# Optimization experiments

Hardware: AMD Instinct MI355X
Metric: run time of the kernel (lower is better)

## Reference

```python
import jax, jax.numpy as jnp
import numpy as np

N_ATOMS = 4096
N_EDGES = 131072
NUM_ELEMENTS = 100
NUM_BESSEL = 8
CUTOFF = 6.0
D_NODE = 64
D_MSG = 128
SH_DIM = 9            # l=0,1,2 -> 1+3+5
TP_IN = D_MSG * SH_DIM  # 1152
N_HEADS = 4
HEAD_DIM = D_MSG // N_HEADS


def setup_inputs() -> dict:
    key = jax.random.key(0)
    ks = jax.random.split(key, 20)
    def p(k, shape):
        return jax.random.normal(k, shape, dtype=jnp.float32) * 0.05
    z = lambda n: jnp.zeros((n,), jnp.float32)
    return {
        "atomic_numbers": jax.random.randint(ks[0], (N_ATOMS,), 0, NUM_ELEMENTS),
        "positions": jax.random.normal(ks[1], (N_ATOMS, 3), dtype=jnp.float32),
        "edge_index": jax.random.randint(ks[2], (2, N_EDGES), 0, N_ATOMS),
        "edge_vectors": jax.random.normal(ks[3], (N_EDGES, 3), dtype=jnp.float32),
        "edge_lengths": jax.random.uniform(ks[4], (N_EDGES,), dtype=jnp.float32, minval=0.5, maxval=5.5),
        "embed_table": p(ks[5], (NUM_ELEMENTS, D_NODE)),
        "W_r1": p(ks[6], (NUM_BESSEL, 64)), "b_r1": z(64),
        "W_r2": p(ks[7], (64, D_MSG)), "b_r2": z(D_MSG),
        "W_tp": p(ks[8], (TP_IN, D_MSG)), "b_tp": z(D_MSG),
        "W_m1": p(ks[9], (D_MSG, D_MSG)), "b_m1": z(D_MSG),
        "W_m2": p(ks[10], (D_MSG, D_MSG)), "b_m2": z(D_MSG),
        "W_qkv": p(ks[11], (D_MSG, 3 * D_MSG)), "b_qkv": z(3 * D_MSG),
        "W_ao": p(ks[12], (D_MSG, D_MSG)), "b_ao": z(D_MSG),
        "W_g": p(ks[13], (D_MSG, D_MSG)), "b_g": z(D_MSG),
        "W_o": p(ks[14], (D_MSG, D_MSG)), "b_o": z(D_MSG),
    }


def reference(atomic_numbers, positions, edge_index, edge_vectors, edge_lengths,
              embed_table, W_r1, b_r1, W_r2, b_r2, W_tp, b_tp,
              W_m1, b_m1, W_m2, b_m2, W_qkv, b_qkv, W_ao, b_ao,
              W_g, b_g, W_o, b_o):
    node_features = embed_table[atomic_numbers]  # [N, 64]

    # spherical harmonics (l = 0,1,2 -> 9 features), order as in source
    r = jnp.linalg.norm(edge_vectors, axis=-1, keepdims=True) + 1e-8
    u = edge_vectors / r
    x, y, z = u[:, 0], u[:, 1], u[:, 2]
    sh = jnp.stack([jnp.ones_like(x), y, z, x,
                    3.0 * z * z - 1.0, x * z, y * z, x * y, x * x - y * y], axis=-1)  # [E,9]

    # bessel RBF with cosine cutoff envelope
    freqs = jnp.arange(1, NUM_BESSEL + 1, dtype=jnp.float32) * (np.pi / CUTOFF)
    env = 0.5 * (jnp.cos(edge_lengths * (np.pi / CUTOFF)) + 1.0) * (edge_lengths < CUTOFF).astype(jnp.float32)
    rbf = jnp.sin(edge_lengths[:, None] * freqs) / edge_lengths[:, None] * env[:, None]  # [E,8]

    radial = jax.nn.silu(rbf @ W_r1 + b_r1)
    radial = jax.nn.silu(radial @ W_r2 + b_r2)  # [E,128]

    # per-edge outer product radial x sh, flattened per-l blocks then concatenated
    outer = radial[:, :, None] * sh[:, None, :]  # [E,128,9]
    E = outer.shape[0]
    edge_messages = jnp.concatenate([
        outer[:, :, 0:1].reshape(E, -1),   # l=0 -> 128
        outer[:, :, 1:4].reshape(E, -1),   # l=1 -> 384
        outer[:, :, 4:9].reshape(E, -1),   # l=2 -> 640
    ], axis=-1)                            # [E,1152]
    edge_messages = edge_messages @ W_tp + b_tp  # [E,128]

    # scatter-add aggregation onto destination nodes (index_add_)
    dst = edge_index[1]
    aggregated = jnp.zeros((node_features.shape[0], D_MSG), jnp.float32).at[dst].add(edge_messages)

    combined = jnp.concatenate([node_features, aggregated[:, :D_NODE]], axis=-1)  # [N,128]
    updated = jax.nn.silu(combined @ W_m1 + b_m1) @ W_m2 + b_m2                   # [N,128]

    # multi-head self-attention over all atoms (batch=1, seq=N)
    N = updated.shape[0]
    qkv = updated @ W_qkv + b_qkv
    q, k, v = jnp.split(qkv, 3, axis=-1)
    q = q.reshape(N, N_HEADS, HEAD_DIM)
    k = k.reshape(N, N_HEADS, HEAD_DIM)
    v = v.reshape(N, N_HEADS, HEAD_DIM)
    scores = jnp.einsum('nhd,mhd->hnm', q, k) / np.sqrt(HEAD_DIM).astype(np.float32)
    attn = jax.nn.softmax(scores, axis=-1)
    attended = jnp.einsum('hnm,mhd->nhd', attn, v).reshape(N, D_MSG)
    attended = attended @ W_ao + b_ao

    gate = jax.nn.sigmoid(updated @ W_g + b_g)
    out = gate * attended + (1.0 - gate) * updated
    return out @ W_o + b_o
```

## Files before the change

### kernel.cpp

```cpp
#include <hip/hip_runtime.h>
#include <hip/hip_bf16.h>
#include <math.h>

#define N_ATOMS 4096
#define N_EDGES 131072
#define PI6 0.52359877559829887308f

typedef __attribute__((ext_vector_type(4))) float f32x4;
typedef _Float16 h16;
typedef __attribute__((ext_vector_type(8))) _Float16 half8;

__device__ __forceinline__ float silu_f(float x) { return x / (1.0f + __expf(-x)); }

__device__ __forceinline__ unsigned pk2h(float lo, float hi) {
    h16 a = (h16)lo, b = (h16)hi;
    unsigned short ua, ub;
    __builtin_memcpy(&ua, &a, 2);
    __builtin_memcpy(&ub, &b, 2);
    return ((unsigned)ub << 16) | (unsigned)ua;
}

__global__ void wprep_kernel(const float* __restrict__ Wtp, float* __restrict__ Wsl)
{
    int idx = blockIdx.x * 256 + threadIdx.x;
    int o = idx & 63;
    int c = (idx >> 6) & 127;
    int s = idx >> 13;
    int row = (s == 0) ? c : (s < 4 ? 128 + c * 3 + (s - 1) : 512 + c * 5 + (s - 4));
    Wsl[idx] = Wtp[row * 128 + o];
}

__global__ void count_kernel(const int* __restrict__ eidx, int* __restrict__ deg)
{
    int e = blockIdx.x * 256 + threadIdx.x;
    atomicAdd(&deg[eidx[N_EDGES + e]], 1);
}

__global__ void scan_kernel(const int* __restrict__ deg, int* __restrict__ base,
                            int* __restrict__ cur)
{
    __shared__ int sums[1024];
    const int t = threadIdx.x;
    int v0 = deg[4*t], v1 = deg[4*t+1], v2 = deg[4*t+2], v3 = deg[4*t+3];
    int s = v0 + v1 + v2 + v3;
    sums[t] = s;
    __syncthreads();
    for (int off = 1; off < 1024; off <<= 1) {
        int x = (t >= off) ? sums[t - off] : 0;
        __syncthreads();
        sums[t] += x;
        __syncthreads();
    }
    int excl = (t > 0) ? sums[t - 1] : 0;
    base[4*t]   = excl;             cur[4*t]   = excl;
    base[4*t+1] = excl + v0;        cur[4*t+1] = excl + v0;
    base[4*t+2] = excl + v0 + v1;   cur[4*t+2] = excl + v0 + v1;
    base[4*t+3] = excl + v0 + v1 + v2; cur[4*t+3] = excl + v0 + v1 + v2;
}

__global__ void scatter_kernel(const int* __restrict__ eidx, int* __restrict__ cur,
                               int* __restrict__ sortedE)
{
    int e = blockIdx.x * 256 + threadIdx.x;
    int dst = eidx[N_EDGES + e];
    int p = atomicAdd(&cur[dst], 1);
    sortedE[p] = e;
}

__global__ __launch_bounds__(256) void agg_kernel(
    const float* __restrict__ evec, const float* __restrict__ elen,
    const int* __restrict__ sortedE, const int* __restrict__ base,
    const int* __restrict__ deg, int aoff,
    const float* __restrict__ Wr1, const float* __restrict__ br1,
    const float* __restrict__ Wr2, const float* __restrict__ br2,
    float* __restrict__ Gm)
{
    __shared__ float rbfL[32][9];
    __shared__ float shL[32][9];
    __shared__ __align__(16) float R1L[64][32];
    __shared__ __align__(16) float R2L[32][128];
    __shared__ __align__(16) float Gh[1152];

    const int t = threadIdx.x;
    const int dst = aoff + blockIdx.x;
    const int dg = deg[dst];
    const int bs = base[dst];

    const int ch = t & 127, hh = t >> 7;
    float G[9] = {0.f,0.f,0.f,0.f,0.f,0.f,0.f,0.f,0.f};

    const int nch = (dg + 31) >> 5;
    for (int c = 0; c < nch; ++c) {
        __syncthreads();
        {
            int el = t >> 3, f = t & 7;
            int ce = c * 32 + el;
            float v = 0.f;
            if (ce < dg) {
                int eid = sortedE[bs + ce];
                float len = elen[eid];
                float env = 0.5f * (cosf(len * PI6) + 1.0f) * (len < 6.0f ? 1.0f : 0.0f);
                v = sinf(len * ((float)(f + 1) * PI6)) * (env / len);
            }
            rbfL[el][f] = v;
        }
        if (t < 32) {
            int ce = c * 32 + t;
            float s0=0,s1=0,s2=0,s3=0,s4=0,s5=0,s6=0,s7=0,s8=0;
            if (ce < dg) {
                int eid = sortedE[bs + ce];
                float vx = evec[eid*3], vy = evec[eid*3+1], vz = evec[eid*3+2];
                float r = sqrtf(vx*vx + vy*vy + vz*vz) + 1e-8f;
                float inv = 1.0f / r;
                float x = vx*inv, y = vy*inv, z = vz*inv;
                s0 = 1.0f; s1 = y; s2 = z; s3 = x;
                s4 = 3.0f*z*z - 1.0f; s5 = x*z; s6 = y*z; s7 = x*y; s8 = x*x - y*y;
            }
            shL[t][0]=s0; shL[t][1]=s1; shL[t][2]=s2; shL[t][3]=s3;
            shL[t][4]=s4; shL[t][5]=s5; shL[t][6]=s6; shL[t][7]=s7; shL[t][8]=s8;
        }
        __syncthreads();
        {
            int e = t & 31, kob = (t >> 5) << 3;
            float rb[8];
            #pragma unroll
            for (int f = 0; f < 8; ++f) rb[f] = rbfL[e][f];
            #pragma unroll
            for (int i = 0; i < 8; ++i) {
                int ko = kob + i;
                float acc = br1[ko];
                #pragma unroll
                for (int f = 0; f < 8; ++f)
                    acc = fmaf(rb[f], Wr1[f * 64 + ko], acc);
                R1L[ko][e] = silu_f(acc);
            }
        }
        __syncthreads();
        {
            int e4 = t >> 5, c4 = t & 31;
            f32x4 a0 = {0.f,0.f,0.f,0.f}, a1 = a0, a2 = a0, a3 = a0;
            const float* Wp = Wr2 + c4 * 4;
            #pragma unroll 4
            for (int j = 0; j < 64; ++j) {
                f32x4 r = *(const f32x4*)&R1L[j][e4 * 4];
                f32x4 w = *(const f32x4*)&Wp[j * 128];
                a0 += w * r.x;
                a1 += w * r.y;
                a2 += w * r.z;
                a3 += w * r.w;
            }
            f32x4 b2 = *(const f32x4*)&br2[c4 * 4];
            a0 += b2; a1 += b2; a2 += b2; a3 += b2;
            f32x4 o0, o1, o2, o3;
            #pragma unroll
            for (int q = 0; q < 4; ++q) {
                o0[q] = silu_f(a0[q]); o1[q] = silu_f(a1[q]);
                o2[q] = silu_f(a2[q]); o3[q] = silu_f(a3[q]);
            }
            *(f32x4*)&R2L[e4*4 + 0][c4*4] = o0;
            *(f32x4*)&R2L[e4*4 + 1][c4*4] = o1;
            *(f32x4*)&R2L[e4*4 + 2][c4*4] = o2;
            *(f32x4*)&R2L[e4*4 + 3][c4*4] = o3;
        }
        __syncthreads();
        {
            int rem = dg - c * 32; if (rem > 32) rem = 32;
            int lo = hh * 16;
            int hi = rem < lo + 16 ? rem : lo + 16;
            for (int el = lo; el < hi; ++el) {
                float r2 = R2L[el][ch];
                #pragma unroll
                for (int s = 0; s < 9; ++s) G[s] = fmaf(shL[el][s], r2, G[s]);
            }
        }
    }

    __syncthreads();
    if (hh == 1) {
        #pragma unroll
        for (int s = 0; s < 9; ++s) Gh[s * 128 + ch] = G[s];
    }
    __syncthreads();
    if (hh == 0) {
        #pragma unroll
        for (int s = 0; s < 9; ++s)
            Gm[blockIdx.x * 1152 + s * 128 + ch] = G[s] + Gh[s * 128 + ch];
    }
}

__global__ __launch_bounds__(256) void gemm_gw_part(
    const float* __restrict__ Gm, const float* __restrict__ Wsl,
    float* __restrict__ P)
{
    __shared__ __align__(16) float AT[128][17];
    __shared__ __align__(16) float Ws[128][64];
    const int t  = threadIdx.x;
    const int M0 = blockIdx.x * 16;
    const int kk = blockIdx.y;

    for (int idx = t; idx < 16 * 128; idx += 256) {
        int m = idx >> 7, k = idx & 127;
        AT[k][m] = Gm[(M0 + m) * 1152 + kk * 128 + k];
    }
    for (int idx = t; idx < 128 * 64; idx += 256) {
        int k = idx >> 6, o = idx & 63;
        Ws[k][o] = Wsl[(kk * 128 + k) * 64 + o];
    }
    __syncthreads();

    const int m0 = t & 15;
    const int o0 = (t >> 4) * 4;
    f32x4 acc = {0.f, 0.f, 0.f, 0.f};
    #pragma unroll 4
    for (int k = 0; k < 128; ++k) {
        float a = AT[k][m0];
        f32x4 w = *(const f32x4*)&Ws[k][o0];
        acc += w * a;
    }
    *(f32x4*)&P[((size_t)kk * 2048 + M0 + m0) * 64 + o0] = acc;
}

__global__ void gw_reduce(const float* __restrict__ P, const int* __restrict__ deg,
                          const float* __restrict__ btp, int aoff,
                          float* __restrict__ agg)
{
    int i = blockIdx.x * 256 + threadIdx.x;
    int m = i >> 6, o = i & 63;
    float s = 0.f;
    #pragma unroll
    for (int kk = 0; kk < 9; ++kk) s += P[(size_t)kk * 131072 + i];
    agg[(aoff + m) * 64 + o] = s + (float)deg[aoff + m] * btp[o];
}

__global__ void combined_kernel(const int* __restrict__ an,
                                const float* __restrict__ emb,
                                const float* __restrict__ agg,
                                float* __restrict__ comb)
{
    int i = blockIdx.x * 256 + threadIdx.x;
    if (i < N_ATOMS * 64) {
        int n = i >> 6, d = i & 63;
        comb[n * 128 + d]      = emb[an[n] * 64 + d];
        comb[n * 128 + 64 + d] = agg[n * 64 + d];
    }
}

template <int ACT>
__global__ __launch_bounds__(256, 2) void gemm128(
    const float* __restrict__ A, const float* __restrict__ W,
    const float* __restrict__ bias, float* __restrict__ C, int N,
    const float* __restrict__ aux1, const float* __restrict__ aux2)
{
    __shared__ __align__(16) float AT[128][64];
    __shared__ __align__(16) float Ws[128][64];
    const int t  = threadIdx.x;
    const int M0 = blockIdx.x * 64;
    const int N0 = blockIdx.y * 64;

    for (int idx = t; idx < 64 * 128; idx += 256) {
        int m = idx >> 7, k = idx & 127;
        AT[k][m ^ ((k & 15) << 2)] = A[(M0 + m) * 128 + k];
    }
    for (int idx = t; idx < 128 * 64; idx += 256) {
        int k = idx >> 6, o = idx & 63;
        Ws[k][o] = W[k * N + N0 + o];
    }
    __syncthreads();

    const int m0 = (t & 15) * 4;
    const int o0 = (t >> 4) * 4;
    float acc[4][4] = {};
    #pragma unroll 2
    for (int k = 0; k < 128; ++k) {
        int xs = (k & 15) << 2;
        float4 a4 = *(const float4*)&AT[k][m0 ^ xs];
        float4 w4 = *(const float4*)&Ws[k][o0];
        float av[4] = {a4.x, a4.y, a4.z, a4.w};
        float wv[4] = {w4.x, w4.y, w4.z, w4.w};
        #pragma unroll
        for (int i = 0; i < 4; ++i)
            #pragma unroll
            for (int j = 0; j < 4; ++j)
                acc[i][j] = fmaf(av[i], wv[j], acc[i][j]);
    }

    #pragma unroll
    for (int i = 0; i < 4; ++i) {
        int m = M0 + m0 + i;
        #pragma unroll
        for (int j = 0; j < 4; ++j) {
            int o = N0 + o0 + j;
            float v = acc[i][j] + bias[o];
            if (ACT == 1) v = silu_f(v);
            if (ACT == 2) {
                float sg = 1.0f / (1.0f + __expf(-v));
                v = sg * aux1[m * 128 + o] + (1.0f - sg) * aux2[m * 128 + o];
            }
            C[m * N + o] = v;
        }
    }
}

__global__ void qkvprep_kernel(const float* __restrict__ qkvf,
                               h16* __restrict__ Qh, h16* __restrict__ Kh,
                               h16* __restrict__ VT)
{
    int i = blockIdx.x * 256 + threadIdx.x;
    {
        int d = i & 31, n = (i >> 5) & 4095, h = i >> 17;
        Qh[i] = (h16)(qkvf[n * 384 + h * 32 + d] * 0.17677669529663687f);
        Kh[i] = (h16)(qkvf[n * 384 + 128 + h * 32 + d]);
    }
    {
        int n = i & 4095, dh = i >> 12;
        VT[i] = (h16)qkvf[n * 384 + 256 + dh];
    }
}

__global__ __launch_bounds__(256, 4) void attn_kernel(
    const h16* __restrict__ Qh, const h16* __restrict__ Kh,
    const h16* __restrict__ VT, float* __restrict__ attd)
{
    __shared__ float st[4][64][10];
    const int t = threadIdx.x, w = t >> 6, lane = t & 63;
    const int h = blockIdx.x >> 8, qt = blockIdx.x & 255;
    const int l15 = lane & 15, g = lane >> 4;

    const h16* Kb = Kh + (size_t)h * 4096 * 32;
    const h16* Vb = VT + (size_t)h * 32 * 4096;
    half8 Qf = *(const half8*)(Qh + ((size_t)(h * 4096 + qt * 16 + l15) * 32 + g * 8));

    float m = -1e30f, l = 0.0f;
    f32x4 O0 = {0.f,0.f,0.f,0.f}, O1 = {0.f,0.f,0.f,0.f};
    const f32x4 zf = {0.f,0.f,0.f,0.f};
    const int sAlane = l15 + ((g & 1) << 5);
    const bool hi = g >= 2;

    const int kvbase = w * 1024;
    for (int kt = 0; kt < 32; ++kt) {
        int kv0 = kvbase + kt * 32;
        half8 K0 = *(const half8*)(Kb + ((size_t)(kv0 + l15) * 32 + g * 8));
        half8 K1 = *(const half8*)(Kb + ((size_t)(kv0 + 16 + l15) * 32 + g * 8));
        f32x4 S0 = __builtin_amdgcn_mfma_f32_16x16x32_f16(K0, Qf, zf, 0, 0, 0);
        f32x4 S1 = __builtin_amdgcn_mfma_f32_16x16x32_f16(K1, Qf, zf, 0, 0, 0);

        float tmax = fmaxf(fmaxf(fmaxf(S0.x, S0.y), fmaxf(S0.z, S0.w)),
                           fmaxf(fmaxf(S1.x, S1.y), fmaxf(S1.z, S1.w)));
        tmax = fmaxf(tmax, __shfl_xor(tmax, 16));
        tmax = fmaxf(tmax, __shfl_xor(tmax, 32));
        float mn = fmaxf(m, tmax);
        float c = __expf(m - mn);
        m = mn;
        float p0[4], p1[4];
        float ts = 0.f;
        #pragma unroll
        for (int i = 0; i < 4; ++i) { p0[i] = __expf(S0[i] - mn); ts += p0[i]; }
        #pragma unroll
        for (int i = 0; i < 4; ++i) { p1[i] = __expf(S1[i] - mn); ts += p1[i]; }
        ts += __shfl_xor(ts, 16);
        ts += __shfl_xor(ts, 32);
        l = l * c + ts;
        #pragma unroll
        for (int i = 0; i < 4; ++i) { O0[i] *= c; O1[i] *= c; }

        unsigned A0 = pk2h(p0[0], p0[1]), A1 = pk2h(p0[2], p0[3]);
        unsigned A2 = pk2h(p1[0], p1[1]), A3 = pk2h(p1[2], p1[3]);
        unsigned t0 = (unsigned)__shfl((int)A0, sAlane);
        unsigned t1 = (unsigned)__shfl((int)A1, sAlane);
        unsigned t2 = (unsigned)__shfl((int)A2, sAlane);
        unsigned t3 = (unsigned)__shfl((int)A3, sAlane);
        unsigned u0 = (unsigned)__shfl((int)A0, sAlane + 16);
        unsigned u1 = (unsigned)__shfl((int)A1, sAlane + 16);
        unsigned u2 = (unsigned)__shfl((int)A2, sAlane + 16);
        unsigned u3 = (unsigned)__shfl((int)A3, sAlane + 16);
        union { unsigned u[4]; half8 v; } P;
        P.u[0] = hi ? t2 : t0;
        P.u[1] = hi ? t3 : t1;
        P.u[2] = hi ? u2 : u0;
        P.u[3] = hi ? u3 : u1;

        half8 V0 = *(const half8*)(Vb + ((size_t)l15 * 4096 + kv0 + g * 8));
        half8 V1 = *(const half8*)(Vb + ((size_t)(16 + l15) * 4096 + kv0 + g * 8));
        O0 = __builtin_amdgcn_mfma_f32_16x16x32_f16(V0, P.v, O0, 0, 0, 0);
        O1 = __builtin_amdgcn_mfma_f32_16x16x32_f16(V1, P.v, O1, 0, 0, 0);
    }

    #pragma unroll
    for (int i = 0; i < 4; ++i) { st[w][lane][i] = O0[i]; st[w][lane][4 + i] = O1[i]; }
    st[w][lane][8] = m;
    st[w][lane][9] = l;
    __syncthreads();

    if (w == 0) {
        float M = -1e30f;
        #pragma unroll
        for (int j = 0; j < 4; ++j) M = fmaxf(M, st[j][lane][8]);
        float L = 0.f, o0[4] = {}, o1[4] = {};
        #pragma unroll
        for (int j = 0; j < 4; ++j) {
            float f = __expf(st[j][lane][8] - M);
            L += st[j][lane][9] * f;
            #pragma unroll
            for (int i = 0; i < 4; ++i) {
                o0[i] = fmaf(st[j][lane][i], f, o0[i]);
                o1[i] = fmaf(st[j][lane][4 + i], f, o1[i]);
            }
        }
        float invL = 1.0f / L;
        int nq = qt * 16 + l15;
        #pragma unroll
        for (int i = 0; i < 4; ++i) {
            attd[nq * 128 + h * 32 + g * 4 + i]      = o0[i] * invL;
            attd[nq * 128 + h * 32 + 16 + g * 4 + i] = o1[i] * invL;
        }
    }
}

extern "C" void kernel_launch(void* const* d_in, const int* in_sizes, int n_in,
                              void* d_out, int out_size, void* d_ws, size_t ws_size,
                              hipStream_t stream) {
    const int*   an    = (const int*)d_in[0];
    const int*   eidx  = (const int*)d_in[2];
    const float* evec  = (const float*)d_in[3];
    const float* elen  = (const float*)d_in[4];
    const float* emb   = (const float*)d_in[5];
    const float* Wr1   = (const float*)d_in[6];
    const float* br1   = (const float*)d_in[7];
    const float* Wr2   = (const float*)d_in[8];
    const float* br2   = (const float*)d_in[9];
    const float* Wtp   = (const float*)d_in[10];
    const float* btp   = (const float*)d_in[11];
    const float* Wm1   = (const float*)d_in[12];
    const float* bm1   = (const float*)d_in[13];
    const float* Wm2   = (const float*)d_in[14];
    const float* bm2   = (const float*)d_in[15];
    const float* Wqkv  = (const float*)d_in[16];
    const float* bqkv  = (const float*)d_in[17];
    const float* Wao   = (const float*)d_in[18];
    const float* bao   = (const float*)d_in[19];
    const float* Wg    = (const float*)d_in[20];
    const float* bg    = (const float*)d_in[21];
    const float* Wo    = (const float*)d_in[22];
    const float* bo    = (const float*)d_in[23];

    float* ws    = (float*)d_ws;
    float* agg   = ws;
    float* comb  = agg  + N_ATOMS * 64;
    float* h1    = comb + N_ATOMS * 128;
    float* upd   = h1   + N_ATOMS * 128;
    float* qkvf  = upd  + N_ATOMS * 128;
    float* attd  = qkvf + N_ATOMS * 384;
    float* aob   = attd + N_ATOMS * 128;
    float* Wsl   = aob;
    int*   deg     = (int*)(aob + 73728);
    int*   base    = deg + 4096;
    int*   cur     = base + 4096;
    int*   sortedE = cur + 4096;
    float* Gm    = comb;
    float* Pp    = ws + 2621440;
    float* outp  = comb;
    h16* Qhb = (h16*)comb;
    h16* Khb = Qhb + 4 * 4096 * 32;
    h16* VTb = (h16*)h1;

    hipMemsetAsync(deg, 0, 4096 * sizeof(int), stream);

    count_kernel<<<512, 256, 0, stream>>>(eidx, deg);
    scan_kernel<<<1, 1024, 0, stream>>>(deg, base, cur);
    scatter_kernel<<<512, 256, 0, stream>>>(eidx, cur, sortedE);

    wprep_kernel<<<288, 256, 0, stream>>>(Wtp, Wsl);

    agg_kernel<<<2048, 256, 0, stream>>>(
        evec, elen, sortedE, base, deg, 0, Wr1, br1, Wr2, br2, Gm);
    gemm_gw_part<<<dim3(128, 9), 256, 0, stream>>>(Gm, Wsl, Pp);
    gw_reduce<<<512, 256, 0, stream>>>(Pp, deg, btp, 0, agg);
    agg_kernel<<<2048, 256, 0, stream>>>(
        evec, elen, sortedE, base, deg, 2048, Wr1, br1, Wr2, br2, Gm);
    gemm_gw_part<<<dim3(128, 9), 256, 0, stream>>>(Gm, Wsl, Pp);
    gw_reduce<<<512, 256, 0, stream>>>(Pp, deg, btp, 2048, agg);

    combined_kernel<<<(N_ATOMS * 64) / 256, 256, 0, stream>>>(an, emb, agg, comb);

    gemm128<1><<<dim3(64, 2), 256, 0, stream>>>(comb, Wm1, bm1, h1, 128, nullptr, nullptr);
    gemm128<0><<<dim3(64, 2), 256, 0, stream>>>(h1, Wm2, bm2, upd, 128, nullptr, nullptr);
    gemm128<0><<<dim3(64, 6), 256, 0, stream>>>(upd, Wqkv, bqkv, qkvf, 384, nullptr, nullptr);

    qkvprep_kernel<<<2048, 256, 0, stream>>>(qkvf, Qhb, Khb, VTb);

    attn_kernel<<<1024, 256, 0, stream>>>(Qhb, Khb, VTb, attd);

    gemm128<0><<<dim3(64, 2), 256, 0, stream>>>(attd, Wao, bao, aob, 128, nullptr, nullptr);
    gemm128<2><<<dim3(64, 2), 256, 0, stream>>>(upd, Wg, bg, outp, 128, aob, upd);
    gemm128<0><<<dim3(64, 2), 256, 0, stream>>>(outp, Wo, bo, (float*)d_out, 128, nullptr, nullptr);
}
```

Before: 315.7 us.

## Fuse edge aggregation with tensor-product projection, four atoms per block

The per-atom edge aggregation kernel now handles four destination atoms per block and multiplies the accumulated 1152-wide features by the sliced W_tp directly in-kernel, adding the degree-scaled bias. This removes the Gm intermediate buffer, the partial GEMM and reduce kernels, and the two-half launch split. The RBF computation is also restructured so one thread per edge computes all eight Bessel sines with a Chebyshev recurrence instead of eight sinf calls. The trade-off is a larger shared-memory footprint, fewer blocks, and a serial 288-step weight loop read from global memory.

```diff
diff --git a/kernel.cpp b/kernel.cpp
--- a/kernel.cpp
+++ b/kernel.cpp
@@ -70,166 +70,151 @@
 __global__ __launch_bounds__(256) void agg_kernel(
     const float* __restrict__ evec, const float* __restrict__ elen,
     const int* __restrict__ sortedE, const int* __restrict__ base,
-    const int* __restrict__ deg, int aoff,
+    const int* __restrict__ deg,
     const float* __restrict__ Wr1, const float* __restrict__ br1,
     const float* __restrict__ Wr2, const float* __restrict__ br2,
-    float* __restrict__ Gm)
+    const float* __restrict__ Wsl, const float* __restrict__ btp,
+    float* __restrict__ agg)
 {
     __shared__ float rbfL[32][9];
     __shared__ float shL[32][9];
     __shared__ __align__(16) float R1L[64][32];
     __shared__ __align__(16) float R2L[32][128];
-    __shared__ __align__(16) float Gh[1152];
+    __shared__ __align__(16) float GL4[4][1152];
+    __shared__ __align__(16) float redL2[4][64][4];
 
     const int t = threadIdx.x;
-    const int dst = aoff + blockIdx.x;
-    const int dg = deg[dst];
-    const int bs = base[dst];
-
     const int ch = t & 127, hh = t >> 7;
-    float G[9] = {0.f,0.f,0.f,0.f,0.f,0.f,0.f,0.f,0.f};
-
-    const int nch = (dg + 31) >> 5;
-    for (int c = 0; c < nch; ++c) {
+
+    for (int a = 0; a < 4; ++a) {
+        const int dst = blockIdx.x * 4 + a;
+        const int dg = deg[dst];
+        const int bs = base[dst];
+        float G[9] = {0.f,0.f,0.f,0.f,0.f,0.f,0.f,0.f,0.f};
+
+        const int nch = (dg + 31) >> 5;
+        for (int c = 0; c < nch; ++c) {
+            __syncthreads();
+            if (t < 32) {
+                int ce = c * 32 + t;
+                float rb[8] = {0.f,0.f,0.f,0.f,0.f,0.f,0.f,0.f};
+                float s0=0,s1=0,s2=0,s3=0,s4=0,s5=0,s6=0,s7=0,s8=0;
+                if (ce < dg) {
+                    int eid = sortedE[bs + ce];
+                    float len = elen[eid];
+                    float th  = len * PI6;
+                    float snt = sinf(th), cst = cosf(th);
+                    float env = 0.5f * (cst + 1.0f) * (len < 6.0f ? 1.0f : 0.0f);
+                    float invl = env / len;
+                    float c2 = 2.0f * cst;
+                    float skm = 0.f, sk = snt;
+                    #pragma unroll
+                    for (int f = 0; f < 8; ++f) {
+                        rb[f] = sk * invl;
+                        float nx = fmaf(c2, sk, -skm);
+                        skm = sk; sk = nx;
+                    }
+                    float vx = evec[eid*3], vy = evec[eid*3+1], vz = evec[eid*3+2];
+                    float r = sqrtf(vx*vx + vy*vy + vz*vz) + 1e-8f;
+                    float inv = 1.0f / r;
+                    float x = vx*inv, y = vy*inv, z = vz*inv;
+                    s0 = 1.0f; s1 = y; s2 = z; s3 = x;
+                    s4 = 3.0f*z*z - 1.0f; s5 = x*z; s6 = y*z; s7 = x*y; s8 = x*x - y*y;
+                }
+                #pragma unroll
+                for (int f = 0; f < 8; ++f) rbfL[t][f] = rb[f];
+                shL[t][0]=s0; shL[t][1]=s1; shL[t][2]=s2; shL[t][3]=s3;
+                shL[t][4]=s4; shL[t][5]=s5; shL[t][6]=s6; shL[t][7]=s7; shL[t][8]=s8;
+            }
+            __syncthreads();
+            {
+                int e = t & 31, kob = (t >> 5) << 3;
+                float rb[8];
+                #pragma unroll
+                for (int f = 0; f < 8; ++f) rb[f] = rbfL[e][f];
+                #pragma unroll
+                for (int i = 0; i < 8; ++i) {
+                    int ko = kob + i;
+                    float acc = br1[ko];
+                    #pragma unroll
+                    for (int f = 0; f < 8; ++f)
+                        acc = fmaf(rb[f], Wr1[f * 64 + ko], acc);
+                    R1L[ko][e] = silu_f(acc);
+                }
+            }
+            __syncthreads();
+            {
+                int e4 = t >> 5, c4 = t & 31;
+                f32x4 a0 = {0.f,0.f,0.f,0.f}, a1 = a0, a2 = a0, a3 = a0;
+                const float* Wp = Wr2 + c4 * 4;
+                #pragma unroll 4
+                for (int j = 0; j < 64; ++j) {
+                    f32x4 r = *(const f32x4*)&R1L[j][e4 * 4];
+                    f32x4 w = *(const f32x4*)&Wp[j * 128];
+                    a0 += w * r.x;
+                    a1 += w * r.y;
+                    a2 += w * r.z;
+                    a3 += w * r.w;
+                }
+                f32x4 b2 = *(const f32x4*)&br2[c4 * 4];
+                a0 += b2; a1 += b2; a2 += b2; a3 += b2;
+                f32x4 o0, o1, o2, o3;
+                #pragma unroll
+                for (int q = 0; q < 4; ++q) {
+                    o0[q] = silu_f(a0[q]); o1[q] = silu_f(a1[q]);
+                    o2[q] = silu_f(a2[q]); o3[q] = silu_f(a3[q]);
+                }
+                *(f32x4*)&R2L[e4*4 + 0][c4*4] = o0;
+                *(f32x4*)&R2L[e4*4 + 1][c4*4] = o1;
+                *(f32x4*)&R2L[e4*4 + 2][c4*4] = o2;
+                *(f32x4*)&R2L[e4*4 + 3][c4*4] = o3;
+            }
+            __syncthreads();
+            {
+                int rem = dg - c * 32; if (rem > 32) rem = 32;
+                int lo = hh * 16;
+                int hi = rem < lo + 16 ? rem : lo + 16;
+                for (int el = lo; el < hi; ++el) {
+                    float r2 = R2L[el][ch];
+                    #pragma unroll
+                    for (int s = 0; s < 9; ++s) G[s] = fmaf(shL[el][s], r2, G[s]);
+                }
+            }
+        }
         __syncthreads();
-        {
-            int el = t >> 3, f = t & 7;
-            int ce = c * 32 + el;
-            float v = 0.f;
-            if (ce < dg) {
-                int eid = sortedE[bs + ce];
-                float len = elen[eid];
-                float env = 0.5f * (cosf(len * PI6) + 1.0f) * (len < 6.0f ? 1.0f : 0.0f);
-                v = sinf(len * ((float)(f + 1) * PI6)) * (env / len);
-            }
-            rbfL[el][f] = v;
-        }
-        if (t < 32) {
-            int ce = c * 32 + t;
-            float s0=0,s1=0,s2=0,s3=0,s4=0,s5=0,s6=0,s7=0,s8=0;
-            if (ce < dg) {
-                int eid = sortedE[bs + ce];
-                float vx = evec[eid*3], vy = evec[eid*3+1], vz = evec[eid*3+2];
-                float r = sqrtf(vx*vx + vy*vy + vz*vz) + 1e-8f;
-                float inv = 1.0f / r;
-                float x = vx*inv, y = vy*inv, z = vz*inv;
-                s0 = 1.0f; s1 = y; s2 = z; s3 = x;
-                s4 = 3.0f*z*z - 1.0f; s5 = x*z; s6 = y*z; s7 = x*y; s8 = x*x - y*y;
-            }
-            shL[t][0]=s0; shL[t][1]=s1; shL[t][2]=s2; shL[t][3]=s3;
-            shL[t][4]=s4; shL[t][5]=s5; shL[t][6]=s6; shL[t][7]=s7; shL[t][8]=s8;
+        if (hh == 1) {
+            #pragma unroll
+            for (int s = 0; s < 9; ++s) GL4[a][s * 128 + ch] = G[s];
         }
         __syncthreads();
-        {
-            int e = t & 31, kob = (t >> 5) << 3;
-            float rb[8];
+        if (hh == 0) {
             #pragma unroll
-            for (int f = 0; f < 8; ++f) rb[f] = rbfL[e][f];
-            #pragma unroll
-            for (int i = 0; i < 8; ++i) {
-                int ko = kob + i;
-                float acc = br1[ko];
-                #pragma unroll
-                for (int f = 0; f < 8; ++f)
-                    acc = fmaf(rb[f], Wr1[f * 64 + ko], acc);
-                R1L[ko][e] = silu_f(acc);
-            }
-        }
-        __syncthreads();
-        {
-            int e4 = t >> 5, c4 = t & 31;
-            f32x4 a0 = {0.f,0.f,0.f,0.f}, a1 = a0, a2 = a0, a3 = a0;
-            const float* Wp = Wr2 + c4 * 4;
-            #pragma unroll 4
-            for (int j = 0; j < 64; ++j) {
-                f32x4 r = *(const f32x4*)&R1L[j][e4 * 4];
-                f32x4 w = *(const f32x4*)&Wp[j * 128];
-                a0 += w * r.x;
-                a1 += w * r.y;
-                a2 += w * r.z;
-                a3 += w * r.w;
-            }
-            f32x4 b2 = *(const f32x4*)&br2[c4 * 4];
-            a0 += b2; a1 += b2; a2 += b2; a3 += b2;
-            f32x4 o0, o1, o2, o3;
-            #pragma unroll
-            for (int q = 0; q < 4; ++q) {
-                o0[q] = silu_f(a0[q]); o1[q] = silu_f(a1[q]);
-                o2[q] = silu_f(a2[q]); o3[q] = silu_f(a3[q]);
-            }
-            *(f32x4*)&R2L[e4*4 + 0][c4*4] = o0;
-            *(f32x4*)&R2L[e4*4 + 1][c4*4] = o1;
-            *(f32x4*)&R2L[e4*4 + 2][c4*4] = o2;
-            *(f32x4*)&R2L[e4*4 + 3][c4*4] = o3;
-        }
-        __syncthreads();
-        {
-            int rem = dg - c * 32; if (rem > 32) rem = 32;
-            int lo = hh * 16;
-            int hi = rem < lo + 16 ? rem : lo + 16;
-            for (int el = lo; el < hi; ++el) {
-                float r2 = R2L[el][ch];
-                #pragma unroll
-                for (int s = 0; s < 9; ++s) G[s] = fmaf(shL[el][s], r2, G[s]);
-            }
+            for (int s = 0; s < 9; ++s) GL4[a][s * 128 + ch] += G[s];
         }
     }
 
     __syncthreads();
-    if (hh == 1) {
-        #pragma unroll
-        for (int s = 0; s < 9; ++s) Gh[s * 128 + ch] = G[s];
+    {
+        const int o = t & 63, qq = t >> 6;
+        f32x4 acc = {0.f, 0.f, 0.f, 0.f};
+        for (int i = 0; i < 288; ++i) {
+            int f = qq * 288 + i;
+            float w = Wsl[f * 64 + o];
+            acc[0] = fmaf(GL4[0][f], w, acc[0]);
+            acc[1] = fmaf(GL4[1][f], w, acc[1]);
+            acc[2] = fmaf(GL4[2][f], w, acc[2]);
+            acc[3] = fmaf(GL4[3][f], w, acc[3]);
+        }
+        *(f32x4*)&redL2[qq][o][0] = acc;
     }
     __syncthreads();
-    if (hh == 0) {
-        #pragma unroll
-        for (int s = 0; s < 9; ++s)
-            Gm[blockIdx.x * 1152 + s * 128 + ch] = G[s] + Gh[s * 128 + ch];
-    }
-}
-
-__global__ __launch_bounds__(256) void gemm_gw_part(
-    const float* __restrict__ Gm, const float* __restrict__ Wsl,
-    float* __restrict__ P)
-{
-    __shared__ __align__(16) float AT[128][17];
-    __shared__ __align__(16) float Ws[128][64];
-    const int t  = threadIdx.x;
-    const int M0 = blockIdx.x * 16;
-    const int kk = blockIdx.y;
-
-    for (int idx = t; idx < 16 * 128; idx += 256) {
-        int m = idx >> 7, k = idx & 127;
-        AT[k][m] = Gm[(M0 + m) * 1152 + kk * 128 + k];
-    }
-    for (int idx = t; idx < 128 * 64; idx += 256) {
-        int k = idx >> 6, o = idx & 63;
-        Ws[k][o] = Wsl[(kk * 128 + k) * 64 + o];
-    }
-    __syncthreads();
-
-    const int m0 = t & 15;
-    const int o0 = (t >> 4) * 4;
-    f32x4 acc = {0.f, 0.f, 0.f, 0.f};
-    #pragma unroll 4
-    for (int k = 0; k < 128; ++k) {
-        float a = AT[k][m0];
-        f32x4 w = *(const f32x4*)&Ws[k][o0];
-        acc += w * a;
-    }
-    *(f32x4*)&P[((size_t)kk * 2048 + M0 + m0) * 64 + o0] = acc;
-}
-
-__global__ void gw_reduce(const float* __restrict__ P, const int* __restrict__ deg,
-                          const float* __restrict__ btp, int aoff,
-                          float* __restrict__ agg)
-{
-    int i = blockIdx.x * 256 + threadIdx.x;
-    int m = i >> 6, o = i & 63;
-    float s = 0.f;
-    #pragma unroll
-    for (int kk = 0; kk < 9; ++kk) s += P[(size_t)kk * 131072 + i];
-    agg[(aoff + m) * 64 + o] = s + (float)deg[aoff + m] * btp[o];
+    {
+        int a2 = t >> 6, o2 = t & 63;
+        float s = redL2[0][o2][a2] + redL2[1][o2][a2]
+                + redL2[2][o2][a2] + redL2[3][o2][a2];
+        int dst = blockIdx.x * 4 + a2;
+        agg[dst * 64 + o2] = s + (float)deg[dst] * btp[o2];
+    }
 }
 
 __global__ void combined_kernel(const int* __restrict__ an,
@@ -456,8 +441,6 @@
     int*   base    = deg + 4096;
     int*   cur     = base + 4096;
     int*   sortedE = cur + 4096;
-    float* Gm    = comb;
-    float* Pp    = ws + 2621440;
     float* outp  = comb;
     h16* Qhb = (h16*)comb;
     h16* Khb = Qhb + 4 * 4096 * 32;
@@ -471,14 +454,8 @@
 
     wprep_kernel<<<288, 256, 0, stream>>>(Wtp, Wsl);
 
-    agg_kernel<<<2048, 256, 0, stream>>>(
-        evec, elen, sortedE, base, deg, 0, Wr1, br1, Wr2, br2, Gm);
-    gemm_gw_part<<<dim3(128, 9), 256, 0, stream>>>(Gm, Wsl, Pp);
-    gw_reduce<<<512, 256, 0, stream>>>(Pp, deg, btp, 0, agg);
-    agg_kernel<<<2048, 256, 0, stream>>>(
-        evec, elen, sortedE, base, deg, 2048, Wr1, br1, Wr2, br2, Gm);
-    gemm_gw_part<<<dim3(128, 9), 256, 0, stream>>>(Gm, Wsl, Pp);
-    gw_reduce<<<512, 256, 0, stream>>>(Pp, deg, btp, 2048, agg);
+    agg_kernel<<<1024, 256, 0, stream>>>(
+        evec, elen, sortedE, base, deg, Wr1, br1, Wr2, br2, Wsl, btp, agg);
 
     combined_kernel<<<(N_ATOMS * 64) / 256, 256, 0, stream>>>(an, emb, agg, comb);
 
```

Result: slower. 352.5 us (+11.6%).
